# Kernel optimization log

Hardware: AMD Instinct MI355X
Metric: run time of the kernel (lower is better)

Reference implementation:

```python
import jax, jax.numpy as jnp
import numpy as np
from jax import lax

B, N, T, E, HE, HD, NE = 512, 100, 100, 128, 64, 256, 512
BETA = 0.25


def setup_inputs() -> dict:
    key = jax.random.key(0)
    ks = jax.random.split(key, 16)
    f32 = jnp.float32
    x = jax.random.normal(ks[0], (B, N, T), f32)
    traj_mask = (jax.random.uniform(ks[1], (B, N, T)) > 0.1).astype(f32)
    instance_mask = (jax.random.uniform(ks[2], (B, N)) > 0.2).astype(f32)

    def w_init(k, shape, fan_in):
        return (jax.random.normal(k, shape, f32) / np.sqrt(fan_in)).astype(f32)

    params = dict(
        conv1_w=w_init(ks[3], (HE, 2, 3), 2 * 3), conv1_b=jnp.zeros((HE,), f32),
        conv2_w=w_init(ks[4], (HE, HE, 3), HE * 3), conv2_b=jnp.zeros((HE,), f32),
        lat_w=w_init(ks[5], (E, HE), HE), lat_b=jnp.zeros((E,), f32),
        codebook=(jax.random.uniform(ks[6], (NE, E), f32) * 2.0 - 1.0) / NE,
        d1_w=w_init(ks[7], (HD, E), E), d1_b=jnp.zeros((HD,), f32),
        d2_w=w_init(ks[8], (HD, HD), HD), d2_b=jnp.zeros((HD,), f32),
        d3_w=w_init(ks[9], (T, HD), HD), d3_b=jnp.zeros((T,), f32),
    )
    return {"x": x, "traj_mask": traj_mask, "instance_mask": instance_mask, **params}


def _conv1d(h, w, b):
    # h: (M, C_in, L), w: (C_out, C_in, K) -> (M, C_out, L), padding=1 == SAME for K=3
    y = lax.conv_general_dilated(h, w, (1,), 'SAME', dimension_numbers=('NCH', 'OIH', 'NCH'))
    return jax.nn.relu(y + b[None, :, None])


def reference(x, traj_mask, instance_mask, conv1_w, conv1_b, conv2_w, conv2_b,
              lat_w, lat_b, codebook, d1_w, d1_b, d2_w, d2_b, d3_w, d3_b):
    b, n, t = x.shape
    steps = t // 2
    im = instance_mask[..., None]  # (B,N,1)

    # ---- encode (masked input) ----
    x_in = x * traj_mask * im
    h = x_in.reshape(b * n, steps, 2).transpose(0, 2, 1)  # (M, 2, steps)
    h = _conv1d(h, conv1_w, conv1_b)
    h = _conv1d(h, conv2_w, conv2_b)
    h = h.mean(axis=-1)                                   # (M, HE)
    z = (h @ lat_w.T + lat_b).reshape(b, n, -1)           # (B, N, E)
    z = z * im

    # ---- vector quantize (nbooks=1), quant_prop=1.0 ----
    zf = z.reshape(-1, z.shape[-1])                       # (M, E)
    d = ((zf * zf).sum(-1, keepdims=True)
         - 2.0 * zf @ codebook.T
         + (codebook * codebook).sum(-1))                 # (M, NE)
    idx = jnp.argmin(d, axis=-1)                          # (M,)
    zq = codebook[idx]                                    # (M, E) gather
    sg = lax.stop_gradient
    vq_loss = (BETA * jnp.mean((zf - sg(zq)) ** 2, -1)
               + jnp.mean((sg(zf) - zq) ** 2, -1)).reshape(b, n)
    zq = zf + sg(zq - zf)                                 # straight-through
    z_q = zq.reshape(b, n, -1)

    # ---- apply instance mask to VQ outputs ----
    denom = jnp.maximum(instance_mask.sum(), 1.0)
    vq_reduced = (vq_loss * instance_mask).sum() / denom
    indices = idx.reshape(b, n, 1)
    indices = jnp.where(im > 0, indices, jnp.full_like(indices, -1))
    z_q = z_q * im

    # ---- decode ----
    h2 = jax.nn.relu(z_q.reshape(b * n, -1) @ d1_w.T + d1_b)
    h2 = jax.nn.relu(h2 @ d2_w.T + d2_b)
    x_hat = (h2 @ d3_w.T + d3_b).reshape(b, n, t)

    # ---- masked reconstruction loss ----
    recon_w = im * traj_mask
    recon_loss = (((x_hat - x) ** 2) * recon_w).sum() / jnp.maximum(recon_w.sum(), 1.0)
    return x_hat, recon_loss, vq_reduced, indices
```

## Files before the change

kernel.cpp:

```cpp
#include <hip/hip_runtime.h>
#include <stdint.h>

typedef unsigned long long u64;
typedef unsigned short ushort_t;
typedef __attribute__((ext_vector_type(8))) short short8;
typedef __attribute__((ext_vector_type(8))) _Float16 half8;
typedef __attribute__((ext_vector_type(16))) float f32x16;

#define VQDEC_BLOCKS 800

#define WS_ENCBHI   6656000ll
#define WS_ENCBLO   6662144ll
#define WS_CBHI     6668288ll
#define WS_CBLO     6701056ll
#define WS_CBNORM   6733824ll
#define WS_D1F      6734336ll
#define WS_D2F      6750720ll
#define WS_D3F      6783488ll
#define WS_RED      6902280ll
#define WS_PART     10179080ll

__device__ __host__ inline ushort_t bf16_rn(float v) {
  unsigned u = __float_as_uint(v);
  unsigned r = (u + 0x7fffu + ((u >> 16) & 1u)) >> 16;
  return (ushort_t)r;
}
union h2u { _Float16 h; unsigned short u; };
union s2h { short8 s; half8 h; };

__device__ inline unsigned pk2_bf16(float a, float b) {
  unsigned r;
  asm("v_cvt_pk_bf16_f32 %0, %1, %2" : "=v"(r) : "v"(a), "v"(b));
  return r;
}

__device__ inline int rowfn(int r, int half) { return (r & 3) + 8*(r >> 2) + 4*half; }

#define MFMA_BF16 __builtin_amdgcn_mfma_f32_32x32x16_bf16
#define MFMA_F16  __builtin_amdgcn_mfma_f32_32x32x16_f16

__global__ __launch_bounds__(256) void prep_kernel(
    const float* __restrict__ w2, const float* __restrict__ cb,
    const float* __restrict__ d1w, const float* __restrict__ d2w,
    const float* __restrict__ d3w,
    ushort_t* __restrict__ ebhi, ushort_t* __restrict__ eblo,
    ushort_t* __restrict__ cbhi, ushort_t* __restrict__ cblo,
    ushort_t* __restrict__ d1f, ushort_t* __restrict__ d2f,
    ushort_t* __restrict__ d3f, float* __restrict__ cbnorm)
{
  const int total = 12288 + 65536 + 32768 + 65536 + 32768 + 512;
  for (int i = blockIdx.x*256 + threadIdx.x; i < total; i += gridDim.x*256) {
    int idx = i;
    if (idx < 12288) {
      int j = idx & 7, l6 = (idx >> 3) & 63, f = idx >> 9;
      int kt = f & 3, ntt = (f >> 2) & 1, t = f >> 3;
      int oc = ntt*32 + (l6 & 31);
      int ic = kt*16 + (l6 >> 5)*8 + j;
      float v = w2[(oc*64 + ic)*3 + t];
      ushort_t hi = bf16_rn(v);
      float hf = __uint_as_float(((unsigned)hi) << 16);
      ebhi[idx] = hi; eblo[idx] = bf16_rn(v - hf); continue;
    }
    idx -= 12288;
    if (idx < 65536) {
      int j = idx & 7, l6 = (idx >> 3) & 63, f = idx >> 9;
      int kt = f & 7, ntg = f >> 3;
      int k = kt*16 + (l6 >> 5)*8 + j;
      int n = ntg*32 + (l6 & 31);
      float v = cb[n*128 + k] * 512.0f;
      h2u a, b; a.h = (_Float16)v;
      b.h = (_Float16)(v - (float)a.h);
      cbhi[idx] = a.u; cblo[idx] = b.u; continue;
    }
    idx -= 65536;
    if (idx < 32768) {
      int j = idx & 7, l6 = (idx >> 3) & 63, f = idx >> 9;
      int kt = f & 7, ntg = f >> 3;
      int k = kt*16 + (l6 >> 5)*8 + j;
      int n = ntg*32 + (l6 & 31);
      d1f[idx] = bf16_rn(d1w[n*128 + k]); continue;
    }
    idx -= 32768;
    if (idx < 65536) {
      int j = idx & 7, l6 = (idx >> 3) & 63, f = idx >> 9;
      int kt = f & 15, ntg = f >> 4;
      int k = kt*16 + (l6 >> 5)*8 + j;
      int n = ntg*32 + (l6 & 31);
      d2f[idx] = bf16_rn(d2w[n*256 + k]); continue;
    }
    idx -= 65536;
    if (idx < 32768) {
      int j = idx & 7, l6 = (idx >> 3) & 63, f = idx >> 9;
      int kt = f & 15, ntg = f >> 4;
      int k = kt*16 + (l6 >> 5)*8 + j;
      int n = ntg*32 + (l6 & 31);
      d3f[idx] = (n < 100) ? bf16_rn(d3w[n*256 + k]) : (ushort_t)0; continue;
    }
    idx -= 32768;
    { double s = 0.0; const float* c = cb + idx*128;
      for (int e = 0; e < 128; ++e) { double v = (double)c[e]; s += v*v; }
      cbnorm[idx] = (float)s; }
  }
}

__global__ __launch_bounds__(256, 3) void encoder_kernel(
    const float* __restrict__ x, const float* __restrict__ tm,
    const float* __restrict__ imask,
    const float* w1, const float* b1,
    const ushort_t* __restrict__ ebhi, const ushort_t* __restrict__ eblo,
    const float* b2, float* __restrict__ red)
{
  __shared__ ushort_t s_H[4][52*128];
  const int tid  = threadIdx.x;
  const int wv   = __builtin_amdgcn_readfirstlane((int)(tid >> 6));
  const int lane = tid & 63;
  const int ln31 = lane & 31, half = lane >> 5;
  const long m   = (long)blockIdx.x*4 + wv;
  const float imv = imask[m];
  ushort_t* Hw  = s_H[wv];

  {
    const int p = (lane < 50) ? lane : 0;
    const long xb = m*100 + 2*p;
    const float2 x0v = *(const float2*)(x + xb);
    const float2 t0v = *(const float2*)(tm + xb);
    float2 xmv = {0.f, 0.f}, tmv = {0.f, 0.f};
    float2 xpv = {0.f, 0.f}, tpv = {0.f, 0.f};
    if (p > 0)  { xmv = *(const float2*)(x + xb - 2); tmv = *(const float2*)(tm + xb - 2); }
    if (p < 49) { xpv = *(const float2*)(x + xb + 2); tpv = *(const float2*)(tm + xb + 2); }
    const float a0 = xmv.x*tmv.x, c0 = xmv.y*tmv.y;
    const float a1 = x0v.x*t0v.x, c1 = x0v.y*t0v.y;
    const float a2 = xpv.x*tpv.x, c2 = xpv.y*tpv.y;
    const int row = lane + 1;
    const int sw  = ((row & 7) << 4) | (((row >> 3) & 1) << 7);
    char* rbase = (char*)(Hw + row*128);
    #pragma unroll
    for (int g = 0; g < 4; ++g) {
      unsigned hi8[8], lo8[8];
      #pragma unroll
      for (int pr = 0; pr < 8; ++pr) {
        const int o = g*16 + pr*2;
        const float* wA = w1 + (long)o*6;
        const float* wB = wA + 6;
        float sA = 0.f, sB = 0.f;
        sA = fmaf(wA[0], a0, sA); sA = fmaf(wA[1], a1, sA); sA = fmaf(wA[2], a2, sA);
        sA = fmaf(wA[3], c0, sA); sA = fmaf(wA[4], c1, sA); sA = fmaf(wA[5], c2, sA);
        sB = fmaf(wB[0], a0, sB); sB = fmaf(wB[1], a1, sB); sB = fmaf(wB[2], a2, sB);
        sB = fmaf(wB[3], c0, sB); sB = fmaf(wB[4], c1, sB); sB = fmaf(wB[5], c2, sB);
        const float hA = fmaxf(fmaf(imv, sA, b1[o]),     0.f);
        const float hB = fmaxf(fmaf(imv, sB, b1[o + 1]), 0.f);
        const unsigned h = pk2_bf16(hA, hB);
        const float ha = __uint_as_float(h << 16);
        const float hb = __uint_as_float(h & 0xffff0000u);
        lo8[pr] = pk2_bf16(hA - ha, hB - hb);
        hi8[pr] = h;
      }
      if (lane < 50) {
        *(short8*)(rbase + ((g*32)        ^ sw)) = *(short8*)&hi8[0];
        *(short8*)(rbase + ((g*32 + 16)   ^ sw)) = *(short8*)&hi8[4];
        *(short8*)(rbase + ((g*32 + 128)  ^ sw)) = *(short8*)&lo8[0];
        *(short8*)(rbase + ((g*32 + 144)  ^ sw)) = *(short8*)&lo8[4];
      }
    }
    if (lane == 50 || lane == 51) {
      const int zr = (lane == 50) ? 0 : 51;
      short8 z8 = {};
      short8* d = (short8*)(Hw + zr*128);
      #pragma unroll
      for (int i = 0; i < 16; ++i) d[i] = z8;
    }
  }
  asm volatile("s_waitcnt lgkmcnt(0)" ::: "memory");
  __builtin_amdgcn_sched_barrier(0);

  f32x16 acc00, acc01, acc10, acc11;
  #pragma unroll
  for (int q = 0; q < 16; ++q) { acc00[q] = 0.f; acc01[q] = 0.f; acc10[q] = 0.f; acc11[q] = 0.f; }
  {
    const short8* bh8 = (const short8*)ebhi;
    const short8* bl8 = (const short8*)eblo;
    for (int t = 0; t < 3; ++t) {
      const int r0 = ln31 + t;
      int r1 = 32 + ln31 + t;
      if (r1 > 51) r1 = 51;
      const int sw0 = ((r0 & 7) << 4) | (((r0 >> 3) & 1) << 7);
      const int sw1 = ((r1 & 7) << 4) | (((r1 >> 3) & 1) << 7);
      const char* b0p = (const char*)(Hw + r0*128);
      const char* b1p = (const char*)(Hw + r1*128);
      #pragma unroll
      for (int kt = 0; kt < 4; ++kt) {
        const int f0 = (t*2 + 0)*4 + kt;
        const int f1 = (t*2 + 1)*4 + kt;
        const int offh = kt*32 + half*16;
        const short8 Bh0 = bh8[f0*64 + lane], Bl0 = bl8[f0*64 + lane];
        const short8 Bh1 = bh8[f1*64 + lane], Bl1 = bl8[f1*64 + lane];
        const short8 ah0 = *(const short8*)(b0p + (offh ^ sw0));
        const short8 al0 = *(const short8*)(b0p + ((offh + 128) ^ sw0));
        const short8 ah1 = *(const short8*)(b1p + (offh ^ sw1));
        const short8 al1 = *(const short8*)(b1p + ((offh + 128) ^ sw1));
        acc00 = MFMA_BF16(ah0, Bh0, acc00, 0, 0, 0);
        acc00 = MFMA_BF16(ah0, Bl0, acc00, 0, 0, 0);
        acc00 = MFMA_BF16(al0, Bh0, acc00, 0, 0, 0);
        acc01 = MFMA_BF16(ah0, Bh1, acc01, 0, 0, 0);
        acc01 = MFMA_BF16(ah0, Bl1, acc01, 0, 0, 0);
        acc01 = MFMA_BF16(al0, Bh1, acc01, 0, 0, 0);
        acc10 = MFMA_BF16(ah1, Bh0, acc10, 0, 0, 0);
        acc10 = MFMA_BF16(ah1, Bl0, acc10, 0, 0, 0);
        acc10 = MFMA_BF16(al1, Bh0, acc10, 0, 0, 0);
        acc11 = MFMA_BF16(ah1, Bh1, acc11, 0, 0, 0);
        acc11 = MFMA_BF16(ah1, Bl1, acc11, 0, 0, 0);
        acc11 = MFMA_BF16(al1, Bh1, acc11, 0, 0, 0);
      }
    }
  }

  {
    const float bv0 = b2[ln31];
    const float bv1 = b2[32 + ln31];
    float s0 = 0.f, s1 = 0.f;
    #pragma unroll
    for (int r = 0; r < 16; ++r) {
      s0 += fmaxf(acc00[r] + bv0, 0.f);
      s1 += fmaxf(acc01[r] + bv1, 0.f);
      const int mpos = 32 + rowfn(r, half);
      const float v10 = fmaxf(acc10[r] + bv0, 0.f);
      const float v11 = fmaxf(acc11[r] + bv1, 0.f);
      if (mpos < 50) { s0 += v10; s1 += v11; }
    }
    s0 += __shfl_xor(s0, 32);
    s1 += __shfl_xor(s1, 32);
    if (half == 0) {
      red[m*64 + ln31]      = s0;
      red[m*64 + 32 + ln31] = s1;
    }
  }
}

__global__ __launch_bounds__(256, 2) void vqdec_kernel(
    const float* __restrict__ red, const float* __restrict__ imask,
    const float* __restrict__ latw, const float* __restrict__ latb,
    const ushort_t* __restrict__ cbhi, const ushort_t* __restrict__ cblo,
    const float* __restrict__ cbnorm, const float* __restrict__ cb,
    const ushort_t* __restrict__ d1frag, const float* __restrict__ d1b,
    const ushort_t* __restrict__ d2frag, const float* __restrict__ d2b,
    const ushort_t* __restrict__ d3frag, const float* __restrict__ d3b,
    const float* __restrict__ x, const float* __restrict__ tm,
    float* __restrict__ xhat, float* __restrict__ out_idx,
    float* __restrict__ pblk)
{
  __shared__ __attribute__((aligned(16))) ushort_t s_reg1[64*264];
  __shared__ __attribute__((aligned(16))) ushort_t s_reg2[64*264];
  __shared__ int s_idx[64];
  __shared__ float s_act[64];
  __shared__ float s_rn0[64], s_rn1[64];
  __shared__ u64 s_best[64];
  __shared__ float s_im[64];
  __shared__ float s_p[4], s_w[4];

  float*    s_r  = (float*)s_reg1;
  ushort_t* s_al = s_reg1 + 8192;
  ushort_t* s_ah = s_reg2;
  ushort_t* s_u  = s_reg1;
  ushort_t* s_h1 = s_reg2;

  const int tid = threadIdx.x;
  const long m0 = (long)blockIdx.x * 64;
  const int wv = tid >> 6, lane = tid & 63;
  const int ln31 = lane & 31, half = lane >> 5;
  float blk_vqp = 0.f, blk_sim = 0.f;

  {
    const int r = tid >> 2, seg = tid & 3;
    const float4* src = (const float4*)(red + (m0 + r)*64 + seg*16);
    float4* dst = (float4*)(s_r + r*64 + seg*16);
    dst[0] = src[0]; dst[1] = src[1]; dst[2] = src[2]; dst[3] = src[3];
  }
  if (tid < 64) { s_im[tid] = imask[m0 + tid]; s_best[tid] = ~0ULL; }
  __syncthreads();

  {
    const int e = tid & 127, mh = tid >> 7;
    float4 W[16];
    const float4* wp = (const float4*)(latw + (long)e*64);
    #pragma unroll
    for (int q = 0; q < 16; ++q) W[q] = wp[q];
    const float lb = latb[e];
    for (int i = 0; i < 32; ++i) {
      const int ml = mh*32 + i;
      const float4* rp = (const float4*)(s_r + ml*64);
      float a0 = 0.f, a1 = 0.f, a2 = 0.f, a3 = 0.f;
      #pragma unroll
      for (int q = 0; q < 16; q += 4) {
        const float4 r0 = rp[q],   r1 = rp[q+1];
        const float4 r2 = rp[q+2], r3 = rp[q+3];
        a0 = fmaf(W[q].x,   r0.x, a0); a0 = fmaf(W[q].y,   r0.y, a0);
        a0 = fmaf(W[q].z,   r0.z, a0); a0 = fmaf(W[q].w,   r0.w, a0);
        a1 = fmaf(W[q+1].x, r1.x, a1); a1 = fmaf(W[q+1].y, r1.y, a1);
        a1 = fmaf(W[q+1].z, r1.z, a1); a1 = fmaf(W[q+1].w, r1.w, a1);
        a2 = fmaf(W[q+2].x, r2.x, a2); a2 = fmaf(W[q+2].y, r2.y, a2);
        a2 = fmaf(W[q+2].z, r2.z, a2); a2 = fmaf(W[q+2].w, r2.w, a2);
        a3 = fmaf(W[q+3].x, r3.x, a3); a3 = fmaf(W[q+3].y, r3.y, a3);
        a3 = fmaf(W[q+3].z, r3.z, a3); a3 = fmaf(W[q+3].w, r3.w, a3);
      }
      const float a = (a0 + a1) + (a2 + a3);
      const float z = fmaf(0.02f, a, lb) * s_im[ml];
      h2u zh, zl; zh.h = (_Float16)z; zl.h = (_Float16)(z - (float)zh.h);
      s_ah[ml*136 + e] = zh.u;
      s_al[ml*136 + e] = zl.u;
      float v = z*z;
      #pragma unroll
      for (int off = 32; off > 0; off >>= 1) v += __shfl_down(v, off);
      if (lane == 0) { if (e < 64) s_rn0[ml] = v; else s_rn1[ml] = v; }
    }
  }
  __syncthreads();

  {
    const short8* ch8 = (const short8*)cbhi;
    const short8* cl8 = (const short8*)cblo;
    #pragma unroll
    for (int mtl = 0; mtl < 2; ++mtl) {
      float rnv[16];
      #pragma unroll
      for (int r = 0; r < 16; ++r) {
        const int g = mtl*32 + rowfn(r, half);
        rnv[r] = s_rn0[g] + s_rn1[g];
      }
      u64 best[16];
      #pragma unroll
      for (int r = 0; r < 16; ++r) best[r] = ~0ULL;
      for (int ct = 0; ct < 4; ++ct) {
        const int ntg = wv*4 + ct;
        half8 Bh[8], Bl[8];
        #pragma unroll
        for (int kt = 0; kt < 8; ++kt) {
          s2h a, b;
          a.s = ch8[(ntg*8 + kt)*64 + lane];
          b.s = cl8[(ntg*8 + kt)*64 + lane];
          Bh[kt] = a.h; Bl[kt] = b.h;
        }
        f32x16 acc;
        #pragma unroll
        for (int q = 0; q < 16; ++q) acc[q] = 0.f;
        const int base8 = (mtl*32 + ln31)*17 + half;
        #pragma unroll
        for (int kt = 0; kt < 8; ++kt) {
          s2h ah, al;
          ah.s = ((const short8*)s_ah)[base8 + kt*2];
          al.s = ((const short8*)s_al)[base8 + kt*2];
          acc = MFMA_F16(ah.h, Bh[kt], acc, 0, 0, 0);
          acc = MFMA_F16(ah.h, Bl[kt], acc, 0, 0, 0);
          acc = MFMA_F16(al.h, Bh[kt], acc, 0, 0, 0);
        }
        const int code = ntg*32 + ln31;
        const float nrm = cbnorm[code];
        #pragma unroll
        for (int r = 0; r < 16; ++r) {
          const float t = fmaf(-0.00390625f, acc[r], rnv[r]);
          const float d = t + nrm;
          const u64 pk = ((u64)__float_as_uint(d) << 32) | (u64)(unsigned)code;
          if (pk < best[r]) best[r] = pk;
        }
      }
      #pragma unroll
      for (int r = 0; r < 16; ++r)
        atomicMin(&s_best[mtl*32 + rowfn(r, half)], best[r]);
    }
  }
  __syncthreads();

  if (tid < 64) {
    const u64 pk = s_best[tid];
    const int ii = (int)(unsigned)(pk & 0xffffffffULL);
    const float dd = __uint_as_float((unsigned)(pk >> 32));
    const float imv = s_im[tid];
    s_idx[tid] = ii; s_act[tid] = imv;
    out_idx[m0 + tid] = (imv > 0.f) ? (float)ii : -1.0f;
    float vqp = 1.25f * dd * (1.0f/128.0f) * imv;
    float sim = imv;
    #pragma unroll
    for (int off = 32; off > 0; off >>= 1) {
      vqp += __shfl_down(vqp, off); sim += __shfl_down(sim, off);
    }
    if (tid == 0) { blk_vqp = vqp; blk_sim = sim; }
  }
  __syncthreads();
  {
    const int row = tid >> 2, seg = tid & 3;
    const float4* src = (const float4*)(cb + (long)s_idx[row]*128 + seg*32);
    const float im = s_act[row];
    ushort_t tmp[32];
    #pragma unroll
    for (int q = 0; q < 8; ++q) {
      const float4 v = src[q];
      tmp[q*4+0] = bf16_rn(v.x*im); tmp[q*4+1] = bf16_rn(v.y*im);
      tmp[q*4+2] = bf16_rn(v.z*im); tmp[q*4+3] = bf16_rn(v.w*im);
    }
    short8* dst = (short8*)(s_u + row*136 + seg*32);
    #pragma unroll
    for (int q = 0; q < 4; ++q) dst[q] = *(short8*)&tmp[q*8];
  }
  __syncthreads();

  {
    const short8* bf = (const short8*)d1frag;
    #pragma unroll
    for (int nti = 0; nti < 2; ++nti) {
      const int ntg = wv + nti*4;
      short8 B[8];
      #pragma unroll
      for (int kt = 0; kt < 8; ++kt) B[kt] = bf[(ntg*8 + kt)*64 + lane];
      const float bv = d1b[ntg*32 + ln31];
      #pragma unroll
      for (int mtl = 0; mtl < 2; ++mtl) {
        f32x16 acc;
        #pragma unroll
        for (int q = 0; q < 16; ++q) acc[q] = 0.f;
        const int base8 = (mtl*32 + ln31)*17 + half;
        #pragma unroll
        for (int kt = 0; kt < 8; ++kt) {
          const short8 a = ((const short8*)s_u)[base8 + kt*2];
          acc = MFMA_BF16(a, B[kt], acc, 0, 0, 0);
        }
        const int col = ntg*32 + ln31;
        #pragma unroll
        for (int r = 0; r < 16; ++r) {
          const int row = mtl*32 + rowfn(r, half);
          s_h1[row*264 + col] = bf16_rn(fmaxf(acc[r] + bv, 0.f));
        }
      }
    }
  }
  __syncthreads();

  {
    const short8* bf = (const short8*)d2frag;
    #pragma unroll
    for (int nti = 0; nti < 2; ++nti) {
      const int ntg = wv + nti*4;
      short8 B[16];
      #pragma unroll
      for (int kt = 0; kt < 16; ++kt) B[kt] = bf[(ntg*16 + kt)*64 + lane];
      const float bv = d2b[ntg*32 + ln31];
      #pragma unroll
      for (int mtl = 0; mtl < 2; ++mtl) {
        f32x16 acc;
        #pragma unroll
        for (int q = 0; q < 16; ++q) acc[q] = 0.f;
        const int base8 = (mtl*32 + ln31)*33 + half;
        #pragma unroll
        for (int kt = 0; kt < 16; ++kt) {
          const short8 a = ((const short8*)s_h1)[base8 + kt*2];
          acc = MFMA_BF16(a, B[kt], acc, 0, 0, 0);
        }
        const int col = ntg*32 + ln31;
        #pragma unroll
        for (int r = 0; r < 16; ++r) {
          const int row = mtl*32 + rowfn(r, half);
          s_u[row*264 + col] = bf16_rn(fmaxf(acc[r] + bv, 0.f));
        }
      }
    }
  }
  __syncthreads();

  {
    const short8* bf = (const short8*)d3frag;
    const int ntg = wv;
    short8 B[16];
    #pragma unroll
    for (int kt = 0; kt < 16; ++kt) B[kt] = bf[(ntg*16 + kt)*64 + lane];
    const int col = ntg*32 + ln31;
    const float bv = (col < 100) ? d3b[col] : 0.f;
    float part = 0.f, wsum = 0.f;
    #pragma unroll
    for (int mtl = 0; mtl < 2; ++mtl) {
      f32x16 acc;
      #pragma unroll
      for (int q = 0; q < 16; ++q) acc[q] = 0.f;
      const int base8 = (mtl*32 + ln31)*33 + half;
      #pragma unroll
      for (int kt = 0; kt < 16; ++kt) {
        const short8 a = ((const short8*)s_u)[base8 + kt*2];
        acc = MFMA_BF16(a, B[kt], acc, 0, 0, 0);
      }
      if (col < 100) {
        #pragma unroll
        for (int r = 0; r < 16; ++r) {
          const long row = m0 + mtl*32 + rowfn(r, half);
          const float xh = acc[r] + bv;
          xhat[row*100 + col] = xh;
          const float wgt = imask[row] * tm[row*100 + col];
          const float df = xh - x[row*100 + col];
          part = fmaf(df*df, wgt, part);
          wsum += wgt;
        }
      }
    }
    #pragma unroll
    for (int off = 32; off > 0; off >>= 1) {
      part += __shfl_down(part, off); wsum += __shfl_down(wsum, off);
    }
    if (lane == 0) { s_p[wv] = part; s_w[wv] = wsum; }
    __syncthreads();
    if (tid == 0) {
      float* p = pblk + (long)blockIdx.x*4;
      p[0] = s_p[0]+s_p[1]+s_p[2]+s_p[3];
      p[1] = blk_vqp;
      p[2] = s_w[0]+s_w[1]+s_w[2]+s_w[3];
      p[3] = blk_sim;
    }
  }
}

__global__ __launch_bounds__(256) void finalize_kernel(
    const float* __restrict__ pblk, float* __restrict__ out)
{
  const int tid = threadIdx.x;
  const int comp = tid >> 6, lane = tid & 63;
  float s = 0.f;
  for (int i = lane; i < VQDEC_BLOCKS; i += 64) s += pblk[i*4 + comp];
  #pragma unroll
  for (int off = 32; off > 0; off >>= 1) s += __shfl_down(s, off);
  __shared__ float sc[4];
  if (lane == 0) sc[comp] = s;
  __syncthreads();
  if (tid == 0) {
    out[5120000] = sc[0] / fmaxf(sc[2], 1.0f);
    out[5120001] = sc[1] / fmaxf(sc[3], 1.0f);
  }
}

extern "C" void kernel_launch(void* const* d_in, const int* in_sizes, int n_in,
                              void* d_out, int out_size, void* d_ws, size_t ws_size,
                              hipStream_t stream)
{
  (void)in_sizes; (void)n_in; (void)out_size; (void)ws_size;
  const float* x     = (const float*)d_in[0];
  const float* tmsk  = (const float*)d_in[1];
  const float* imask = (const float*)d_in[2];
  const float* w1    = (const float*)d_in[3];
  const float* b1    = (const float*)d_in[4];
  const float* w2    = (const float*)d_in[5];
  const float* b2    = (const float*)d_in[6];
  const float* latw  = (const float*)d_in[7];
  const float* latb  = (const float*)d_in[8];
  const float* cb    = (const float*)d_in[9];
  const float* d1w   = (const float*)d_in[10];
  const float* d1b   = (const float*)d_in[11];
  const float* d2w   = (const float*)d_in[12];
  const float* d2b   = (const float*)d_in[13];
  const float* d3w   = (const float*)d_in[14];
  const float* d3b   = (const float*)d_in[15];
  float* out = (float*)d_out;
  float* ws  = (float*)d_ws;

  ushort_t* ebhi   = (ushort_t*)(ws + WS_ENCBHI);
  ushort_t* eblo   = (ushort_t*)(ws + WS_ENCBLO);
  ushort_t* cbhi   = (ushort_t*)(ws + WS_CBHI);
  ushort_t* cblo   = (ushort_t*)(ws + WS_CBLO);
  float*    cbnorm = ws + WS_CBNORM;
  ushort_t* d1f    = (ushort_t*)(ws + WS_D1F);
  ushort_t* d2f    = (ushort_t*)(ws + WS_D2F);
  ushort_t* d3f    = (ushort_t*)(ws + WS_D3F);
  float*    red    = ws + WS_RED;
  float*    pblk   = ws + WS_PART;
  float* xhat    = out;
  float* out_idx = out + 5120002;

  prep_kernel<<<512, 256, 0, stream>>>(w2, cb, d1w, d2w, d3w,
                                       ebhi, eblo, cbhi, cblo, d1f, d2f, d3f, cbnorm);
  encoder_kernel<<<12800, 256, 0, stream>>>(x, tmsk, imask, w1, b1, ebhi, eblo, b2, red);
  vqdec_kernel<<<VQDEC_BLOCKS, 256, 0, stream>>>(red, imask, latw, latb, cbhi, cblo,
                                                 cbnorm, cb, d1f, d1b, d2f, d2b,
                                                 d3f, d3b, x, tmsk, xhat, out_idx, pblk);
  finalize_kernel<<<1, 256, 0, stream>>>(pblk, out);
}
```

Measured before the change: 423.5 us.

## Split weight prep and fold non-encoder prep into encoder grid

Weight preparation is split in two. A tiny kernel now converts only the encoder conv2 weights. The codebook, decoder-weight and codebook-norm conversion runs in extra blocks appended to the encoder launch, so it overlaps with encoder work rather than serializing before it. This removes most of the standalone prep kernel's latency. In exchange there is a still-serial tiny launch, and the tail blocks now use the encoder's shared-memory footprint, which may reduce their occupancy.

```diff
diff --git a/kernel.cpp b/kernel.cpp
--- a/kernel.cpp
+++ b/kernel.cpp
@@ -8,6 +8,8 @@
 typedef __attribute__((ext_vector_type(16))) float f32x16;
 
 #define VQDEC_BLOCKS 800
+#define ENC_BLOCKS   12800
+#define PREP_BLOCKS  512
 
 #define WS_ENCBHI   6656000ll
 #define WS_ENCBLO   6662144ll
@@ -39,29 +41,32 @@
 #define MFMA_BF16 __builtin_amdgcn_mfma_f32_32x32x16_bf16
 #define MFMA_F16  __builtin_amdgcn_mfma_f32_32x32x16_f16
 
-__global__ __launch_bounds__(256) void prep_kernel(
-    const float* __restrict__ w2, const float* __restrict__ cb,
+__global__ __launch_bounds__(256) void prep_enc_kernel(
+    const float* __restrict__ w2,
+    ushort_t* __restrict__ ebhi, ushort_t* __restrict__ eblo)
+{
+  const int idx = blockIdx.x*256 + threadIdx.x;
+  int j = idx & 7, l6 = (idx >> 3) & 63, f = idx >> 9;
+  int kt = f & 3, ntt = (f >> 2) & 1, t = f >> 3;
+  int oc = ntt*32 + (l6 & 31);
+  int ic = kt*16 + (l6 >> 5)*8 + j;
+  float v = w2[(oc*64 + ic)*3 + t];
+  ushort_t hi = bf16_rn(v);
+  float hf = __uint_as_float(((unsigned)hi) << 16);
+  ebhi[idx] = hi; eblo[idx] = bf16_rn(v - hf);
+}
+
+__device__ void prep_rest(int pb, int tid,
+    const float* __restrict__ cb,
     const float* __restrict__ d1w, const float* __restrict__ d2w,
     const float* __restrict__ d3w,
-    ushort_t* __restrict__ ebhi, ushort_t* __restrict__ eblo,
     ushort_t* __restrict__ cbhi, ushort_t* __restrict__ cblo,
     ushort_t* __restrict__ d1f, ushort_t* __restrict__ d2f,
     ushort_t* __restrict__ d3f, float* __restrict__ cbnorm)
 {
-  const int total = 12288 + 65536 + 32768 + 65536 + 32768 + 512;
-  for (int i = blockIdx.x*256 + threadIdx.x; i < total; i += gridDim.x*256) {
+  const int total = 65536 + 32768 + 65536 + 32768 + 512;
+  for (int i = pb*256 + tid; i < total; i += PREP_BLOCKS*256) {
     int idx = i;
-    if (idx < 12288) {
-      int j = idx & 7, l6 = (idx >> 3) & 63, f = idx >> 9;
-      int kt = f & 3, ntt = (f >> 2) & 1, t = f >> 3;
-      int oc = ntt*32 + (l6 & 31);
-      int ic = kt*16 + (l6 >> 5)*8 + j;
-      float v = w2[(oc*64 + ic)*3 + t];
-      ushort_t hi = bf16_rn(v);
-      float hf = __uint_as_float(((unsigned)hi) << 16);
-      ebhi[idx] = hi; eblo[idx] = bf16_rn(v - hf); continue;
-    }
-    idx -= 12288;
     if (idx < 65536) {
       int j = idx & 7, l6 = (idx >> 3) & 63, f = idx >> 9;
       int kt = f & 7, ntg = f >> 3;
@@ -108,10 +113,21 @@
     const float* __restrict__ imask,
     const float* w1, const float* b1,
     const ushort_t* __restrict__ ebhi, const ushort_t* __restrict__ eblo,
-    const float* b2, float* __restrict__ red)
+    const float* b2, float* __restrict__ red,
+    const float* __restrict__ cb,
+    const float* __restrict__ d1w, const float* __restrict__ d2w,
+    const float* __restrict__ d3w,
+    ushort_t* __restrict__ cbhi, ushort_t* __restrict__ cblo,
+    ushort_t* __restrict__ d1f, ushort_t* __restrict__ d2f,
+    ushort_t* __restrict__ d3f, float* __restrict__ cbnorm)
 {
   __shared__ ushort_t s_H[4][52*128];
   const int tid  = threadIdx.x;
+  if (blockIdx.x >= ENC_BLOCKS) {
+    prep_rest((int)blockIdx.x - ENC_BLOCKS, tid, cb, d1w, d2w, d3w,
+              cbhi, cblo, d1f, d2f, d3f, cbnorm);
+    return;
+  }
   const int wv   = __builtin_amdgcn_readfirstlane((int)(tid >> 6));
   const int lane = tid & 63;
   const int ln31 = lane & 31, half = lane >> 5;
@@ -568,9 +584,10 @@
   float* xhat    = out;
   float* out_idx = out + 5120002;
 
-  prep_kernel<<<512, 256, 0, stream>>>(w2, cb, d1w, d2w, d3w,
-                                       ebhi, eblo, cbhi, cblo, d1f, d2f, d3f, cbnorm);
-  encoder_kernel<<<12800, 256, 0, stream>>>(x, tmsk, imask, w1, b1, ebhi, eblo, b2, red);
+  prep_enc_kernel<<<48, 256, 0, stream>>>(w2, ebhi, eblo);
+  encoder_kernel<<<ENC_BLOCKS + PREP_BLOCKS, 256, 0, stream>>>(
+      x, tmsk, imask, w1, b1, ebhi, eblo, b2, red,
+      cb, d1w, d2w, d3w, cbhi, cblo, d1f, d2f, d3f, cbnorm);
   vqdec_kernel<<<VQDEC_BLOCKS, 256, 0, stream>>>(red, imask, latw, latb, cbhi, cblo,
                                                  cbnorm, cb, d1f, d1b, d2f, d2b,
                                                  d3f, d3b, x, tmsk, xhat, out_idx, pblk);
```

Result: no change. 417.0 us (-1.5%).
